# Optimization experiments

Hardware: AMD Instinct MI355X
Metric: run time of the kernel (lower is better)

## Reference

```python
import jax, jax.numpy as jnp
import numpy as np

B, T, C, A, D, H, W = 2, 16, 64, 64, 32, 32, 32  # batch, timepoints, channels, att_features, spatial


def setup_inputs() -> dict:
    key = jax.random.key(0)
    ks = jax.random.split(key, 7)
    s = 1.0 / np.sqrt(C)
    return {
        "x": jax.random.normal(ks[0], (B, T, C, D, H, W), dtype=jnp.float32),
        "Wk": jax.random.normal(ks[1], (A, C), dtype=jnp.float32) * s,
        "bk": jax.random.normal(ks[2], (A,), dtype=jnp.float32) * s,
        "Wq": jax.random.normal(ks[3], (A, C), dtype=jnp.float32) * s,
        "bq": jax.random.normal(ks[4], (A,), dtype=jnp.float32) * s,
        "Wv": jax.random.normal(ks[5], (C, C), dtype=jnp.float32) * s,
        "bv": jax.random.normal(ks[6], (C,), dtype=jnp.float32) * s,
    }


def reference(x, Wk, bk, Wq, bq, Wv, bv):
    # kernel=1 Conv3d == pointwise channel mixing. Project and move spatial
    # dims to the front exactly like movedim((3,4,5),(1,2,3)):
    # result layout [B, D, H, W, T, out_ch].
    def proj(Wt, bt):
        return jnp.einsum('btcdhw,oc->bdhwto', x, Wt) + bt

    k = proj(Wk, bk)  # [B,D,H,W,T,A]
    q = proj(Wq, bq)  # [B,D,H,W,T,A]
    v = proj(Wv, bv)  # [B,D,H,W,T,C]

    scale = 1.0 / np.sqrt(float(Wk.shape[0]))  # sqrt(att_features)
    att = jnp.einsum('bdhwta,bdhwsa->bdhwts', k, q) * scale  # [B,D,H,W,T,T]
    # norm = partial(softmax, dim=1) on the 6-D tensor -> softmax over spatial D axis
    att_map = jax.nn.softmax(att, axis=1)

    # features = (value^T @ att_map)^T: feat[...,s,c] = sum_t v[...,t,c] * att_map[...,t,s]
    feat = jnp.einsum('bdhwtc,bdhwts->bdhwsc', v, att_map)  # [B,D,H,W,T,C]
    # movedim((1,2,3),(3,4,5)): back to [B, T, C, D, H, W]
    return jnp.transpose(feat, (0, 4, 5, 1, 2, 3))
```

## Files before the change

### kernel.cpp

```cpp
#include <hip/hip_runtime.h>

typedef short v8s __attribute__((ext_vector_type(8)));
typedef float v4f __attribute__((ext_vector_type(4)));
typedef float v2f __attribute__((ext_vector_type(2)));

#define NSP 32768
#define ZOFF 8192
#define XSTR 2056
#define FSTR 34

__device__ __forceinline__ unsigned short f2bf(float f) {
  union { float f; unsigned u; } v; v.f = f;
  unsigned r = v.u + 0x7fffu + ((v.u >> 16) & 1u);
  return (unsigned short)(r >> 16);
}
__device__ __forceinline__ unsigned pk(float a, float b) {
  return (unsigned)f2bf(a) | ((unsigned)f2bf(b) << 16);
}

union UF8 { v8s v; unsigned u[4]; uint4 q; };


__global__ __launch_bounds__(512) void prep_kernel(
    const float* __restrict__ Wk, const float* __restrict__ bk,
    const float* __restrict__ Wq, const float* __restrict__ bq,
    const float* __restrict__ Wv, unsigned* __restrict__ ws) {
  __shared__ float sWk[4096], sWq[4096], sWv[4096], sbk[64], sbq[64];
  for (int i = threadIdx.x; i < 4096; i += 512) { sWk[i] = Wk[i]; sWq[i] = Wq[i]; sWv[i] = Wv[i]; }
  if (threadIdx.x < 64) { sbk[threadIdx.x] = bk[threadIdx.x]; sbq[threadIdx.x] = bq[threadIdx.x]; }
  __syncthreads();
  for (int task = threadIdx.x; task < 18 * 64; task += 512) {
    int f = task >> 6, lane = task & 63;
    int i16 = lane & 15, g = lane >> 4;
    unsigned short e[8];
    #pragma unroll
    for (int j = 0; j < 8; ++j) {
      int k = (((j >> 2) << 4) + 4 * g + (j & 3));
      float acc = 0.f;
      if (f < 8) {
        int row = ((f >> 1) << 4) + i16;
        int cc  = ((f & 1) << 5) + k;
        for (int a = 0; a < 64; ++a) acc += sWk[a * 64 + row] * sWq[a * 64 + cc];
      } else if (f < 10) {
        int c = ((f - 8) << 5) + k;
        if (i16 == 0)      { for (int a = 0; a < 64; ++a) acc += sWk[a * 64 + c] * sbq[a]; }
        else if (i16 == 1) { for (int a = 0; a < 64; ++a) acc += sbk[a] * sWq[a * 64 + c]; }
      } else {
        int c  = (((f - 10) >> 1) << 4) + i16;
        int cp = (((f - 10) & 1) << 5) + k;
        acc = sWv[c * 64 + cp];
      }
      e[j] = f2bf(acc);
    }
    unsigned* dst = ws + (size_t)(f * 64 + lane) * 4;
    dst[0] = e[0] | ((unsigned)e[1] << 16);
    dst[1] = e[2] | ((unsigned)e[3] << 16);
    dst[2] = e[4] | ((unsigned)e[5] << 16);
    dst[3] = e[6] | ((unsigned)e[7] << 16);
  }
  if (threadIdx.x == 0) {
    float beta = 0.f;
    for (int a = 0; a < 64; ++a) beta += sbk[a] * sbq[a];
    ((float*)ws)[18 * 256] = beta;
  }
}

#define S2L 0.18033688011112042f

#define DECODE_GRID() \
  int bid = (int)blockIdx.x; \
  int b = bid & 1, dc = (bid >> 1) & 3, h = bid >> 3; \
  const int d0 = dc << 3; \
  const size_t base0 = (size_t)b * 33554432 + h * 32;

#define STAGE_DEFS() \
  const int w2 = tid & 15; \
  const int rp0 = tid >> 4; \
  v2f sA[16], sB[16]; \
  auto issueRegs = [&](int d) { \
    const float* xp = x + base0 + (size_t)d * 1024; \
    _Pragma("unroll") \
    for (int i = 0; i < 16; ++i) { \
      int rp = (i << 5) + rp0; \
      const float* r0 = xp + (size_t)(2 * rp) * NSP + 2 * w2; \
      sA[i] = *(const v2f*)r0; \
      sB[i] = *(const v2f*)(r0 + NSP); \
    } \
  }; \
  auto writeLds = [&]() { \
    _Pragma("unroll") \
    for (int i = 0; i < 16; ++i) { \
      int rp = (i << 5) + rp0; \
      int t = rp >> 5, c = (rp & 31) << 1; \
      int off = (t << 7) + (((c << 1)) ^ ((t & 7) << 4)); \
      *(unsigned*)(&Xbuf[(2 * w2) * XSTR + off])     = pk(sA[i].x, sB[i].x); \
      *(unsigned*)(&Xbuf[(2 * w2 + 1) * XSTR + off]) = pk(sA[i].y, sB[i].y); \
    } \
  };

#define LOADX_DEF() \
  auto loadX = [&](int loc, v8s fX[2]) { \
    const unsigned char* bp = &Xbuf[loc * XSTR + (i16 << 7)]; \
    const int sw = (i16 & 7) << 4; \
    _Pragma("unroll") \
    for (int kc = 0; kc < 2; ++kc) { \
      union { v8s v; unsigned long long dd[2]; } u; \
      int o = (kc << 6) + (g << 3); \
      u.dd[0] = *(const unsigned long long*)(bp + (o ^ sw)); \
      u.dd[1] = *(const unsigned long long*)(bp + ((o + 32) ^ sw)); \
      fX[kc] = u.v; \
    } \
  };

#define ATTOF_DEF() \
  auto attOf = [&](const v8s fX[2]) -> v4f { \
    v4f accW[4]; \
    _Pragma("unroll") \
    for (int tr = 0; tr < 4; ++tr) { \
      v4f a = {0.f, 0.f, 0.f, 0.f}; \
      a = __builtin_amdgcn_mfma_f32_16x16x32_bf16(fM[tr][0], fX[0], a, 0, 0, 0); \
      a = __builtin_amdgcn_mfma_f32_16x16x32_bf16(fM[tr][1], fX[1], a, 0, 0, 0); \
      accW[tr] = a; \
    } \
    v4f au = {0.f, 0.f, 0.f, 0.f}; \
    au = __builtin_amdgcn_mfma_f32_16x16x32_bf16(fUR[0], fX[0], au, 0, 0, 0); \
    au = __builtin_amdgcn_mfma_f32_16x16x32_bf16(fUR[1], fX[1], au, 0, 0, 0); \
    float a1v = au[0] + beta; \
    float a2v = au[1]; \
    float a2s = __shfl(a2v, i16); \
    v4f att; \
    _Pragma("unroll") \
    for (int j = 0; j < 4; ++j) att[j] = __shfl(a1v, 4 * g + j) + a2s; \
    _Pragma("unroll") \
    for (int kc = 0; kc < 2; ++kc) { \
      UF8 w; \
      w.u[0] = pk(accW[2 * kc][0], accW[2 * kc][1]); \
      w.u[1] = pk(accW[2 * kc][2], accW[2 * kc][3]); \
      w.u[2] = pk(accW[2 * kc + 1][0], accW[2 * kc + 1][1]); \
      w.u[3] = pk(accW[2 * kc + 1][2], accW[2 * kc + 1][3]); \
      att = __builtin_amdgcn_mfma_f32_16x16x32_bf16(fX[kc], w.v, att, 0, 0, 0); \
    } \
    return att; \
  };

__global__ __launch_bounds__(512) void pass1_z(
    const float* __restrict__ x, const unsigned* __restrict__ ws,
    float* __restrict__ zp) {
  __shared__ __align__(16) unsigned char Xbuf[32 * XSTR];

  const int tid = (int)threadIdx.x;
  const int lane = tid & 63, wv = tid >> 6;
  const int i16 = lane & 15, g = lane >> 4;
  DECODE_GRID();

  v8s fM[4][2], fUR[2];
  {
    const uint4* W4 = (const uint4*)ws;
    #pragma unroll
    for (int f = 0; f < 8; ++f) { UF8 u; u.q = W4[f * 64 + lane]; fM[f >> 1][f & 1] = u.v; }
    #pragma unroll
    for (int f = 0; f < 2; ++f) { UF8 u; u.q = W4[(8 + f) * 64 + lane]; fUR[f] = u.v; }
  }
  const float beta = ((const float*)ws)[4608];

  STAGE_DEFS();
  LOADX_DEF();
  ATTOF_DEF();

  float Z[4][4] = {};
  issueRegs(d0);
  for (int ii = 0; ii < 8; ++ii) {
    __syncthreads();
    writeLds();
    if (ii < 7) issueRegs(d0 + ii + 1);
    __syncthreads();
    #pragma unroll
    for (int l = 0; l < 4; ++l) {
      v8s fX[2]; loadX(4 * wv + l, fX);
      v4f att = attOf(fX);
      #pragma unroll
      for (int j = 0; j < 4; ++j) Z[l][j] += exp2f(att[j] * S2L);
    }
  }
  const int locg = b * 1024 + h * 32 + 4 * wv;
  #pragma unroll
  for (int l = 0; l < 4; ++l)
    #pragma unroll
    for (int j = 0; j < 4; ++j)
      zp[(((size_t)dc * 2048 + locg + l) << 8) + (4 * g + j) * 16 + i16] = Z[l][j];
}

__global__ __launch_bounds__(512) void pass2_out(
    const float* __restrict__ x, const float* __restrict__ bv,
    const unsigned* __restrict__ ws, const float* __restrict__ zp,
    float* __restrict__ out) {
  __shared__ __align__(16) unsigned char Xbuf[32 * XSTR];
  __shared__ float Fb[512 * FSTR];

  const int tid = (int)threadIdx.x;
  const int lane = tid & 63, wv = tid >> 6;
  const int i16 = lane & 15, g = lane >> 4;
  DECODE_GRID();

  v8s fM[4][2], fUR[2], fWv[4][2];
  {
    const uint4* W4 = (const uint4*)ws;
    #pragma unroll
    for (int f = 0; f < 8; ++f) { UF8 u; u.q = W4[f * 64 + lane]; fM[f >> 1][f & 1] = u.v; }
    #pragma unroll
    for (int f = 0; f < 2; ++f) { UF8 u; u.q = W4[(8 + f) * 64 + lane]; fUR[f] = u.v; }
    #pragma unroll
    for (int f = 0; f < 8; ++f) { UF8 u; u.q = W4[(10 + f) * 64 + lane]; fWv[f >> 1][f & 1] = u.v; }
  }
  const float beta = ((const float*)ws)[4608];
  float bvv[4];
  #pragma unroll
  for (int tn = 0; tn < 4; ++tn) bvv[tn] = bv[i16 + 16 * tn];

  const int locg = b * 1024 + h * 32 + 4 * wv;
  float iZ[4][4];
  #pragma unroll
  for (int l = 0; l < 4; ++l)
    #pragma unroll
    for (int j = 0; j < 4; ++j) {
      float s = 0.f;
      #pragma unroll
      for (int c2 = 0; c2 < 4; ++c2)
        s += zp[(((size_t)c2 * 2048 + locg + l) << 8) + (4 * g + j) * 16 + i16];
      iZ[l][j] = 1.f / s;
    }

  STAGE_DEFS();
  LOADX_DEF();
  ATTOF_DEF();

  auto storeHalf = [&](int half, int d) {
    float* op = out + base0 + (size_t)d * 1024 + ((size_t)half << 5) * NSP;
    const int w4 = tid & 7, rr = tid >> 3;
    #pragma unroll
    for (int ro = 0; ro < 8; ++ro) {
      int r = (ro << 6) + rr;
      int s = r >> 5, ci = r & 31;
      int v = ((r >> 7) & 1) << 2;
      int bse = r * FSTR + ((w4 << 2) ^ v);
      float4 val;
      val.x = Fb[bse]; val.y = Fb[bse + 1]; val.z = Fb[bse + 2]; val.w = Fb[bse + 3];
      *(float4*)(op + (size_t)(s * 64 + ci) * NSP + (w4 << 2)) = val;
    }
  };

  issueRegs(d0 + 7);
  for (int ii = 0; ii < 8; ++ii) {
    const int d = d0 + 7 - ii;
    __syncthreads();
    writeLds();
    if (ii < 7) issueRegs(d - 1);
    __syncthreads();

    unsigned fPs[4][2];
    #pragma unroll
    for (int l = 0; l < 4; ++l) {
      const int w = 4 * wv + l;
      v8s fX[2]; loadX(w, fX);
      v4f att = attOf(fX);
      float p[4];
      #pragma unroll
      for (int j = 0; j < 4; ++j) p[j] = exp2f(att[j] * S2L) * iZ[l][j];
      fPs[l][0] = pk(p[0], p[1]); fPs[l][1] = pk(p[2], p[3]);
      #pragma unroll
      for (int tn = 0; tn < 2; ++tn) {
        v4f a = {bvv[tn], bvv[tn], bvv[tn], bvv[tn]};
        a = __builtin_amdgcn_mfma_f32_16x16x32_bf16(fX[0], fWv[tn][0], a, 0, 0, 0);
        a = __builtin_amdgcn_mfma_f32_16x16x32_bf16(fX[1], fWv[tn][1], a, 0, 0, 0);
        UF8 fV; fV.u[0] = pk(a[0], a[1]); fV.u[1] = pk(a[2], a[3]); fV.u[2] = 0; fV.u[3] = 0;
        UF8 fP; fP.u[0] = fPs[l][0]; fP.u[1] = fPs[l][1]; fP.u[2] = 0; fP.u[3] = 0;
        v4f ft = {0.f, 0.f, 0.f, 0.f};
        ft = __builtin_amdgcn_mfma_f32_16x16x32_bf16(fP.v, fV.v, ft, 0, 0, 0);
        #pragma unroll
        for (int j = 0; j < 4; ++j) {
          int r = (4 * g + j) * 32 + i16 + 16 * tn;
          Fb[r * FSTR + (w ^ (((r >> 7) & 1) << 2))] = ft[j];
        }
      }
    }
    __syncthreads();
    storeHalf(0, d);
    __syncthreads();
    #pragma unroll
    for (int l = 0; l < 4; ++l) {
      const int w = 4 * wv + l;
      v8s fX[2]; loadX(w, fX);
      #pragma unroll
      for (int tn = 2; tn < 4; ++tn) {
        v4f a = {bvv[tn], bvv[tn], bvv[tn], bvv[tn]};
        a = __builtin_amdgcn_mfma_f32_16x16x32_bf16(fX[0], fWv[tn][0], a, 0, 0, 0);
        a = __builtin_amdgcn_mfma_f32_16x16x32_bf16(fX[1], fWv[tn][1], a, 0, 0, 0);
        UF8 fV; fV.u[0] = pk(a[0], a[1]); fV.u[1] = pk(a[2], a[3]); fV.u[2] = 0; fV.u[3] = 0;
        UF8 fP; fP.u[0] = fPs[l][0]; fP.u[1] = fPs[l][1]; fP.u[2] = 0; fP.u[3] = 0;
        v4f ft = {0.f, 0.f, 0.f, 0.f};
        ft = __builtin_amdgcn_mfma_f32_16x16x32_bf16(fP.v, fV.v, ft, 0, 0, 0);
        #pragma unroll
        for (int j = 0; j < 4; ++j) {
          int r = (4 * g + j) * 32 + i16 + 16 * (tn - 2);
          Fb[r * FSTR + (w ^ (((r >> 7) & 1) << 2))] = ft[j];
        }
      }
    }
    __syncthreads();
    storeHalf(1, d);
  }
}

extern "C" void kernel_launch(void* const* d_in, const int* in_sizes, int n_in,
                              void* d_out, int out_size, void* d_ws, size_t ws_size,
                              hipStream_t stream) {
  const float* x  = (const float*)d_in[0];
  const float* Wk = (const float*)d_in[1];
  const float* bk = (const float*)d_in[2];
  const float* Wq = (const float*)d_in[3];
  const float* bq = (const float*)d_in[4];
  const float* Wv = (const float*)d_in[5];
  const float* bv = (const float*)d_in[6];
  float* out = (float*)d_out;
  unsigned* ws = (unsigned*)d_ws;
  float* zp = (float*)d_ws + ZOFF;

  prep_kernel<<<1, 512, 0, stream>>>(Wk, bk, Wq, bq, Wv, ws);
  pass1_z<<<256, 512, 0, stream>>>(x, ws, zp);
  pass2_out<<<256, 512, 0, stream>>>(x, bv, ws, zp, out);
}
```

Baseline: 322.3 us.

## Double grid to 512 blocks, move weights to LDS, overlap feature stores

Both passes now launch 512 blocks, each covering 4 depth slices instead of 8, so every CU has more blocks. The bf16 weight fragments move from registers into shared memory, and Wv fragments are re-read from global memory inside the loop, which frees VGPRs. Staging loads are split into halves. In pass2 the feature output is produced in four quarter tiles ping-ponged between two LDS buffers aliased onto the X buffer, so stores of one quarter overlap computation of the next. The cost is extra LDS reads per MFMA, a second zp reduction over 8 partials, and more barriers.

```diff
diff --git a/kernel.cpp b/kernel.cpp
--- a/kernel.cpp
+++ b/kernel.cpp
@@ -5,9 +5,8 @@
 typedef float v2f __attribute__((ext_vector_type(2)));
 
 #define NSP 32768
-#define ZOFF 8192
 #define XSTR 2056
-#define FSTR 34
+#define WS_ZP_B 65536ull
 
 __device__ __forceinline__ unsigned short f2bf(float f) {
   union { float f; unsigned u; } v; v.f = f;
@@ -67,40 +66,40 @@
 
 #define S2L 0.18033688011112042f
 
-#define DECODE_GRID() \
+#define DECODE512() \
   int bid = (int)blockIdx.x; \
-  int b = bid & 1, dc = (bid >> 1) & 3, h = bid >> 3; \
-  const int d0 = dc << 3; \
+  int b = bid & 1, dcc = (bid >> 1) & 7, h = bid >> 4; \
+  const int d0 = dcc << 2; \
   const size_t base0 = (size_t)b * 33554432 + h * 32;
 
-#define STAGE_DEFS() \
+#define STAGE_DEFS(BUF) \
   const int w2 = tid & 15; \
   const int rp0 = tid >> 4; \
-  v2f sA[16], sB[16]; \
-  auto issueRegs = [&](int d) { \
+  v2f sA[8], sB[8]; \
+  auto issueH = [&](int d, int half) { \
     const float* xp = x + base0 + (size_t)d * 1024; \
     _Pragma("unroll") \
-    for (int i = 0; i < 16; ++i) { \
-      int rp = (i << 5) + rp0; \
+    for (int i = 0; i < 8; ++i) { \
+      int rp = half * 256 + (i << 5) + rp0; \
       const float* r0 = xp + (size_t)(2 * rp) * NSP + 2 * w2; \
       sA[i] = *(const v2f*)r0; \
       sB[i] = *(const v2f*)(r0 + NSP); \
     } \
   }; \
-  auto writeLds = [&]() { \
-    _Pragma("unroll") \
-    for (int i = 0; i < 16; ++i) { \
-      int rp = (i << 5) + rp0; \
+  auto writeH = [&](int half) { \
+    _Pragma("unroll") \
+    for (int i = 0; i < 8; ++i) { \
+      int rp = half * 256 + (i << 5) + rp0; \
       int t = rp >> 5, c = (rp & 31) << 1; \
       int off = (t << 7) + (((c << 1)) ^ ((t & 7) << 4)); \
-      *(unsigned*)(&Xbuf[(2 * w2) * XSTR + off])     = pk(sA[i].x, sB[i].x); \
-      *(unsigned*)(&Xbuf[(2 * w2 + 1) * XSTR + off]) = pk(sA[i].y, sB[i].y); \
-    } \
-  };
-
-#define LOADX_DEF() \
+      *(unsigned*)(&BUF[(2 * w2) * XSTR + off])     = pk(sA[i].x, sB[i].x); \
+      *(unsigned*)(&BUF[(2 * w2 + 1) * XSTR + off]) = pk(sA[i].y, sB[i].y); \
+    } \
+  };
+
+#define LOADX_DEF(BUF) \
   auto loadX = [&](int loc, v8s fX[2]) { \
-    const unsigned char* bp = &Xbuf[loc * XSTR + (i16 << 7)]; \
+    const unsigned char* bp = &BUF[loc * XSTR + (i16 << 7)]; \
     const int sw = (i16 & 7) << 4; \
     _Pragma("unroll") \
     for (int kc = 0; kc < 2; ++kc) { \
@@ -112,19 +111,28 @@
     } \
   };
 
+#define LDF_DEF() \
+  auto ldf = [&](int f) -> v8s { \
+    union { v8s v; uint4 q; } u; \
+    u.q = *(const uint4*)&Wm[(f << 8) + (lane << 2)]; \
+    return u.v; \
+  };
+
 #define ATTOF_DEF() \
   auto attOf = [&](const v8s fX[2]) -> v4f { \
     v4f accW[4]; \
     _Pragma("unroll") \
     for (int tr = 0; tr < 4; ++tr) { \
+      v8s m0 = ldf(2 * tr), m1 = ldf(2 * tr + 1); \
       v4f a = {0.f, 0.f, 0.f, 0.f}; \
-      a = __builtin_amdgcn_mfma_f32_16x16x32_bf16(fM[tr][0], fX[0], a, 0, 0, 0); \
-      a = __builtin_amdgcn_mfma_f32_16x16x32_bf16(fM[tr][1], fX[1], a, 0, 0, 0); \
+      a = __builtin_amdgcn_mfma_f32_16x16x32_bf16(m0, fX[0], a, 0, 0, 0); \
+      a = __builtin_amdgcn_mfma_f32_16x16x32_bf16(m1, fX[1], a, 0, 0, 0); \
       accW[tr] = a; \
     } \
+    v8s u0 = ldf(8), u1 = ldf(9); \
     v4f au = {0.f, 0.f, 0.f, 0.f}; \
-    au = __builtin_amdgcn_mfma_f32_16x16x32_bf16(fUR[0], fX[0], au, 0, 0, 0); \
-    au = __builtin_amdgcn_mfma_f32_16x16x32_bf16(fUR[1], fX[1], au, 0, 0, 0); \
+    au = __builtin_amdgcn_mfma_f32_16x16x32_bf16(u0, fX[0], au, 0, 0, 0); \
+    au = __builtin_amdgcn_mfma_f32_16x16x32_bf16(u1, fX[1], au, 0, 0, 0); \
     float a1v = au[0] + beta; \
     float a2v = au[1]; \
     float a2s = __shfl(a2v, i16); \
@@ -143,37 +151,51 @@
     return att; \
   };
 
+#define FEATQ(tn, FB) do { \
+  _Pragma("unroll") \
+  for (int l = 0; l < 4; ++l) { \
+    int wq = 4 * wv + l; \
+    UF8 fP; fP.u[0] = Pp[l][0]; fP.u[1] = Pp[l][1]; fP.u[2] = 0; fP.u[3] = 0; \
+    UF8 fV; fV.u[0] = vp[l][2 * (tn)]; fV.u[1] = vp[l][2 * (tn) + 1]; fV.u[2] = 0; fV.u[3] = 0; \
+    v4f ft = {0.f, 0.f, 0.f, 0.f}; \
+    ft = __builtin_amdgcn_mfma_f32_16x16x32_bf16(fP.v, fV.v, ft, 0, 0, 0); \
+    _Pragma("unroll") \
+    for (int j = 0; j < 4; ++j) { \
+      int r = (4 * g + j) * 16 + i16; \
+      (FB)[r * 33 + (wq ^ g)] = ft[j]; \
+    } \
+  } \
+} while (0)
+
 __global__ __launch_bounds__(512) void pass1_z(
     const float* __restrict__ x, const unsigned* __restrict__ ws,
     float* __restrict__ zp) {
   __shared__ __align__(16) unsigned char Xbuf[32 * XSTR];
+  __shared__ unsigned Wm[2560];
 
   const int tid = (int)threadIdx.x;
   const int lane = tid & 63, wv = tid >> 6;
   const int i16 = lane & 15, g = lane >> 4;
-  DECODE_GRID();
-
-  v8s fM[4][2], fUR[2];
-  {
-    const uint4* W4 = (const uint4*)ws;
-    #pragma unroll
-    for (int f = 0; f < 8; ++f) { UF8 u; u.q = W4[f * 64 + lane]; fM[f >> 1][f & 1] = u.v; }
-    #pragma unroll
-    for (int f = 0; f < 2; ++f) { UF8 u; u.q = W4[(8 + f) * 64 + lane]; fUR[f] = u.v; }
-  }
+  DECODE512();
+
+  for (int o = tid; o < 2560; o += 512) Wm[o] = ws[o];
   const float beta = ((const float*)ws)[4608];
 
-  STAGE_DEFS();
-  LOADX_DEF();
+  STAGE_DEFS(Xbuf);
+  LOADX_DEF(Xbuf);
+  LDF_DEF();
   ATTOF_DEF();
 
   float Z[4][4] = {};
-  issueRegs(d0);
-  for (int ii = 0; ii < 8; ++ii) {
-    __syncthreads();
-    writeLds();
-    if (ii < 7) issueRegs(d0 + ii + 1);
-    __syncthreads();
+  issueH(d0, 0);
+  for (int ii = 0; ii < 4; ++ii) {
+    const int d = d0 + ii;
+    __syncthreads();
+    writeH(0);
+    issueH(d, 1);
+    writeH(1);
+    __syncthreads();
+    if (ii < 3) issueH(d + 1, 0);
     #pragma unroll
     for (int l = 0; l < 4; ++l) {
       v8s fX[2]; loadX(4 * wv + l, fX);
@@ -187,127 +209,105 @@
   for (int l = 0; l < 4; ++l)
     #pragma unroll
     for (int j = 0; j < 4; ++j)
-      zp[(((size_t)dc * 2048 + locg + l) << 8) + (4 * g + j) * 16 + i16] = Z[l][j];
+      zp[(((size_t)dcc * 2048 + locg + l) << 8) + (4 * g + j) * 16 + i16] = Z[l][j];
 }
 
 __global__ __launch_bounds__(512) void pass2_out(
     const float* __restrict__ x, const float* __restrict__ bv,
     const unsigned* __restrict__ ws, const float* __restrict__ zp,
     float* __restrict__ out) {
-  __shared__ __align__(16) unsigned char Xbuf[32 * XSTR];
-  __shared__ float Fb[512 * FSTR];
+  __shared__ __align__(16) unsigned char UNI[67584];
+  __shared__ unsigned Wm[2560];
 
   const int tid = (int)threadIdx.x;
   const int lane = tid & 63, wv = tid >> 6;
   const int i16 = lane & 15, g = lane >> 4;
-  DECODE_GRID();
-
-  v8s fM[4][2], fUR[2], fWv[4][2];
-  {
-    const uint4* W4 = (const uint4*)ws;
-    #pragma unroll
-    for (int f = 0; f < 8; ++f) { UF8 u; u.q = W4[f * 64 + lane]; fM[f >> 1][f & 1] = u.v; }
-    #pragma unroll
-    for (int f = 0; f < 2; ++f) { UF8 u; u.q = W4[(8 + f) * 64 + lane]; fUR[f] = u.v; }
-    #pragma unroll
-    for (int f = 0; f < 8; ++f) { UF8 u; u.q = W4[(10 + f) * 64 + lane]; fWv[f >> 1][f & 1] = u.v; }
-  }
+  DECODE512();
+
+  for (int o = tid; o < 2560; o += 512) Wm[o] = ws[o];
   const float beta = ((const float*)ws)[4608];
   float bvv[4];
   #pragma unroll
   for (int tn = 0; tn < 4; ++tn) bvv[tn] = bv[i16 + 16 * tn];
 
-  const int locg = b * 1024 + h * 32 + 4 * wv;
   float iZ[4][4];
   #pragma unroll
-  for (int l = 0; l < 4; ++l)
+  for (int l = 0; l < 4; ++l) {
+    const int locg = b * 1024 + h * 32 + 4 * wv + l;
     #pragma unroll
     for (int j = 0; j < 4; ++j) {
       float s = 0.f;
       #pragma unroll
-      for (int c2 = 0; c2 < 4; ++c2)
-        s += zp[(((size_t)c2 * 2048 + locg + l) << 8) + (4 * g + j) * 16 + i16];
+      for (int c2 = 0; c2 < 8; ++c2)
+        s += zp[(((size_t)c2 * 2048 + locg) << 8) + (4 * g + j) * 16 + i16];
       iZ[l][j] = 1.f / s;
     }
-
-  STAGE_DEFS();
-  LOADX_DEF();
+  }
+
+  STAGE_DEFS(UNI);
+  LOADX_DEF(UNI);
+  LDF_DEF();
   ATTOF_DEF();
 
-  auto storeHalf = [&](int half, int d) {
-    float* op = out + base0 + (size_t)d * 1024 + ((size_t)half << 5) * NSP;
+  float* FbA = (float*)UNI;
+  float* FbB = FbA + 8448;
+  const uint4* W4 = (const uint4*)ws;
+
+  auto storeQ = [&](int tn, int d, const float* FB) {
+    float* op = out + base0 + (size_t)d * 1024 + (size_t)(16 * tn) * NSP;
     const int w4 = tid & 7, rr = tid >> 3;
     #pragma unroll
-    for (int ro = 0; ro < 8; ++ro) {
-      int r = (ro << 6) + rr;
-      int s = r >> 5, ci = r & 31;
-      int v = ((r >> 7) & 1) << 2;
-      int bse = r * FSTR + ((w4 << 2) ^ v);
+    for (int it = 0; it < 4; ++it) {
+      int r = (it << 6) + rr;
+      const float* fp = &FB[r * 33 + (w4 << 2)];
       float4 val;
-      val.x = Fb[bse]; val.y = Fb[bse + 1]; val.z = Fb[bse + 2]; val.w = Fb[bse + 3];
-      *(float4*)(op + (size_t)(s * 64 + ci) * NSP + (w4 << 2)) = val;
-    }
-  };
-
-  issueRegs(d0 + 7);
-  for (int ii = 0; ii < 8; ++ii) {
-    const int d = d0 + 7 - ii;
-    __syncthreads();
-    writeLds();
-    if (ii < 7) issueRegs(d - 1);
-    __syncthreads();
-
-    unsigned fPs[4][2];
+      val.x = fp[0 ^ it]; val.y = fp[1 ^ it]; val.z = fp[2 ^ it]; val.w = fp[3 ^ it];
+      *(float4*)(op + (size_t)((r >> 4) * 64 + (r & 15)) * NSP + (w4 << 2)) = val;
+    }
+  };
+
+  issueH(d0, 0);
+  for (int ii = 0; ii < 4; ++ii) {
+    const int d = d0 + ii;
+    __syncthreads();
+    writeH(0);
+    issueH(d, 1);
+    writeH(1);
+    __syncthreads();
+    if (ii < 3) issueH(d + 1, 0);
+
+    unsigned Pp[4][2], vp[4][8];
     #pragma unroll
     for (int l = 0; l < 4; ++l) {
-      const int w = 4 * wv + l;
-      v8s fX[2]; loadX(w, fX);
+      v8s fX[2]; loadX(4 * wv + l, fX);
       v4f att = attOf(fX);
-      float p[4];
+      float p0 = exp2f(att[0] * S2L) * iZ[l][0];
+      float p1 = exp2f(att[1] * S2L) * iZ[l][1];
+      float p2 = exp2f(att[2] * S2L) * iZ[l][2];
+      float p3 = exp2f(att[3] * S2L) * iZ[l][3];
+      Pp[l][0] = pk(p0, p1); Pp[l][1] = pk(p2, p3);
       #pragma unroll
-      for (int j = 0; j < 4; ++j) p[j] = exp2f(att[j] * S2L) * iZ[l][j];
-      fPs[l][0] = pk(p[0], p[1]); fPs[l][1] = pk(p[2], p[3]);
-      #pragma unroll
-      for (int tn = 0; tn < 2; ++tn) {
+      for (int tn = 0; tn < 4; ++tn) {
+        UF8 wa, wb;
+        wa.q = W4[(10 + 2 * tn) * 64 + lane];
+        wb.q = W4[(11 + 2 * tn) * 64 + lane];
         v4f a = {bvv[tn], bvv[tn], bvv[tn], bvv[tn]};
-        a = __builtin_amdgcn_mfma_f32_16x16x32_bf16(fX[0], fWv[tn][0], a, 0, 0, 0);
-        a = __builtin_amdgcn_mfma_f32_16x16x32_bf16(fX[1], fWv[tn][1], a, 0, 0, 0);
-        UF8 fV; fV.u[0] = pk(a[0], a[1]); fV.u[1] = pk(a[2], a[3]); fV.u[2] = 0; fV.u[3] = 0;
-        UF8 fP; fP.u[0] = fPs[l][0]; fP.u[1] = fPs[l][1]; fP.u[2] = 0; fP.u[3] = 0;
-        v4f ft = {0.f, 0.f, 0.f, 0.f};
-        ft = __builtin_amdgcn_mfma_f32_16x16x32_bf16(fP.v, fV.v, ft, 0, 0, 0);
-        #pragma unroll
-        for (int j = 0; j < 4; ++j) {
-          int r = (4 * g + j) * 32 + i16 + 16 * tn;
-          Fb[r * FSTR + (w ^ (((r >> 7) & 1) << 2))] = ft[j];
-        }
+        a = __builtin_amdgcn_mfma_f32_16x16x32_bf16(fX[0], wa.v, a, 0, 0, 0);
+        a = __builtin_amdgcn_mfma_f32_16x16x32_bf16(fX[1], wb.v, a, 0, 0, 0);
+        vp[l][2 * tn] = pk(a[0], a[1]); vp[l][2 * tn + 1] = pk(a[2], a[3]);
       }
     }
     __syncthreads();
-    storeHalf(0, d);
-    __syncthreads();
-    #pragma unroll
-    for (int l = 0; l < 4; ++l) {
-      const int w = 4 * wv + l;
-      v8s fX[2]; loadX(w, fX);
-      #pragma unroll
-      for (int tn = 2; tn < 4; ++tn) {
-        v4f a = {bvv[tn], bvv[tn], bvv[tn], bvv[tn]};
-        a = __builtin_amdgcn_mfma_f32_16x16x32_bf16(fX[0], fWv[tn][0], a, 0, 0, 0);
-        a = __builtin_amdgcn_mfma_f32_16x16x32_bf16(fX[1], fWv[tn][1], a, 0, 0, 0);
-        UF8 fV; fV.u[0] = pk(a[0], a[1]); fV.u[1] = pk(a[2], a[3]); fV.u[2] = 0; fV.u[3] = 0;
-        UF8 fP; fP.u[0] = fPs[l][0]; fP.u[1] = fPs[l][1]; fP.u[2] = 0; fP.u[3] = 0;
-        v4f ft = {0.f, 0.f, 0.f, 0.f};
-        ft = __builtin_amdgcn_mfma_f32_16x16x32_bf16(fP.v, fV.v, ft, 0, 0, 0);
-        #pragma unroll
-        for (int j = 0; j < 4; ++j) {
-          int r = (4 * g + j) * 32 + i16 + 16 * (tn - 2);
-          Fb[r * FSTR + (w ^ (((r >> 7) & 1) << 2))] = ft[j];
-        }
-      }
-    }
-    __syncthreads();
-    storeHalf(1, d);
+
+    FEATQ(0, FbA);
+    __syncthreads();
+    storeQ(0, d, FbA); FEATQ(1, FbB);
+    __syncthreads();
+    storeQ(1, d, FbB); FEATQ(2, FbA);
+    __syncthreads();
+    storeQ(2, d, FbA); FEATQ(3, FbB);
+    __syncthreads();
+    storeQ(3, d, FbB);
   }
 }
 
@@ -323,9 +323,9 @@
   const float* bv = (const float*)d_in[6];
   float* out = (float*)d_out;
   unsigned* ws = (unsigned*)d_ws;
-  float* zp = (float*)d_ws + ZOFF;
+  float* zp = (float*)((char*)d_ws + WS_ZP_B);
 
   prep_kernel<<<1, 512, 0, stream>>>(Wk, bk, Wq, bq, Wv, ws);
-  pass1_z<<<256, 512, 0, stream>>>(x, ws, zp);
-  pass2_out<<<256, 512, 0, stream>>>(x, bv, ws, zp, out);
-}
+  pass1_z<<<512, 512, 0, stream>>>(x, ws, zp);
+  pass2_out<<<512, 512, 0, stream>>>(x, bv, ws, zp, out);
+}
```

After: 298.0 us. 7.6% less time.
